# Kernel optimization log

Hardware: AMD Instinct MI355X
Metric: run time of the kernel (lower is better)

## Reference

```python
import jax, jax.numpy as jnp
import numpy as np

NEG_SLOPE = 0.2  # PyG GATv2Conv default negative_slope


def segment_softmax(scores, dst, num_nodes):
    # scores: [E, H], softmax over edges sharing the same destination node
    m = jax.ops.segment_max(scores, dst, num_segments=num_nodes)  # [N, H]
    e = jnp.exp(scores - m[dst])
    s = jax.ops.segment_sum(e, dst, num_segments=num_nodes)  # [N, H]
    return e / (s[dst] + 1e-16)


def gatv2_conv(x, src, dst, Wl, bl, Wr, br, att, bias, heads, out_ch, concat):
    # PyG GATv2: x_l = lin_l(x) used for source/messages, x_r = lin_r(x) for target
    n = x.shape[0]
    xl = (x @ Wl + bl).reshape(n, heads, out_ch)
    xr = (x @ Wr + br).reshape(n, heads, out_ch)
    e = jax.nn.leaky_relu(xl[src] + xr[dst], NEG_SLOPE)        # [E, H, C]
    score = jnp.einsum('ehc,hc->eh', e, att)                    # [E, H]
    alpha = segment_softmax(score, dst, n)                      # [E, H]
    msg = xl[src] * alpha[..., None]                            # [E, H, C]
    out = jax.ops.segment_sum(msg, dst, num_segments=n)         # [N, H, C]
    out = out.reshape(n, heads * out_ch) if concat else out.mean(axis=1)
    return out + bias


def setup_inputs() -> dict:
    key = jax.random.key(0)
    ks = jax.random.split(key, 20)
    N, F_IN, H, C = 50000, 256, 4, 64
    E = 600000
    x = jax.random.normal(ks[0], (N, F_IN), dtype=jnp.float32)
    edge_index = jax.random.randint(ks[1], (2, E), 0, N, dtype=jnp.int64)

    def glorot(k, shape):
        fan_in = shape[0]
        return jax.random.normal(k, shape, dtype=jnp.float32) / jnp.sqrt(jnp.float32(fan_in))

    params = dict(
        # layer 1: in=256, heads=4, out=64, concat -> 256
        W1l=glorot(ks[2], (F_IN, H * C)), b1l=jnp.zeros((H * C,), jnp.float32),
        W1r=glorot(ks[3], (F_IN, H * C)), b1r=jnp.zeros((H * C,), jnp.float32),
        att1=glorot(ks[4], (H, C)), bias1=jnp.zeros((H * C,), jnp.float32),
        # layer 2: in=256, heads=1, out=64, no concat
        W2l=glorot(ks[5], (H * C, C)), b2l=jnp.zeros((C,), jnp.float32),
        W2r=glorot(ks[6], (H * C, C)), b2r=jnp.zeros((C,), jnp.float32),
        att2=glorot(ks[7], (1, C)), bias2=jnp.zeros((C,), jnp.float32),
        # predict head: 64 -> 32 -> 1
        Wp1=glorot(ks[8], (C, 32)), bp1=jnp.zeros((32,), jnp.float32),
        Wp2=glorot(ks[9], (32, 1)), bp2=jnp.zeros((1,), jnp.float32),
    )
    return {'x': x, 'edge_index': edge_index, **params}


def reference(x, edge_index, W1l, b1l, W1r, b1r, att1, bias1,
              W2l, b2l, W2r, b2r, att2, bias2, Wp1, bp1, Wp2, bp2):
    n = x.shape[0]
    # PyG GATv2Conv default add_self_loops=True
    loop = jnp.arange(n, dtype=edge_index.dtype)
    src = jnp.concatenate([edge_index[0], loop])
    dst = jnp.concatenate([edge_index[1], loop])

    h = gatv2_conv(x, src, dst, W1l, b1l, W1r, b1r, att1, bias1,
                   heads=4, out_ch=64, concat=True)
    h = jax.nn.leaky_relu(h, 0.01)  # F.leaky_relu default slope
    h = gatv2_conv(h, src, dst, W2l, b2l, W2r, b2r, att2, bias2,
                   heads=1, out_ch=64, concat=False)
    z = jax.nn.leaky_relu(h @ Wp1 + bp1, 0.01)
    logits = z @ Wp2 + bp2
    return logits, h
```

## Files before the change

### kernel.cpp

```cpp
#include <hip/hip_runtime.h>

typedef __attribute__((ext_vector_type(8))) __bf16 bf16x8;
typedef __attribute__((ext_vector_type(4))) float f32x4;

#define EXP2 __builtin_amdgcn_exp2f
#define LOG2E 1.44269504f
#define MFMA __builtin_amdgcn_mfma_f32_16x16x32_bf16

#define GLL(srcp, dstp) __builtin_amdgcn_global_load_lds( \
    (const __attribute__((address_space(1))) void*)(srcp), \
    (__attribute__((address_space(3))) void*)(dstp), 16, 0, 0)

__device__ __forceinline__ float lrelu(float v, float s) { return v > 0.f ? v : v * s; }

__device__ __forceinline__ unsigned short f2bf(float f) {
    unsigned int u = __float_as_uint(f);
    u += 0x7FFFu + ((u >> 16) & 1u);
    return (unsigned short)(u >> 16);
}
__device__ __forceinline__ float bf2f(unsigned short u) {
    return __uint_as_float((unsigned int)u << 16);
}

__device__ __forceinline__ int ld_idx(const int* p, int e, int is64) {
    return is64 ? (int)(((const long long*)p)[e]) : p[e];
}

__global__ void detect_i64(const unsigned int* idx, int* flag) {
    if (blockIdx.x == 0 && threadIdx.x == 0) {
        int all0 = 1;
        for (int i = 1; i < 256; i += 2) {
            if (idx[i] != 0u) { all0 = 0; break; }
        }
        *flag = all0;
    }
}

__global__ void convert_all(const float* __restrict__ x,
                            const float* __restrict__ W1l, const float* __restrict__ W1r,
                            const float* __restrict__ W2l, const float* __restrict__ W2r,
                            unsigned short* __restrict__ xb,
                            unsigned short* __restrict__ w1t, unsigned short* __restrict__ w2t,
                            int n, int nrb)
{
    int t = blockIdx.x * blockDim.x + threadIdx.x;
    int A = nrb * 512;
    if (t < A) {
        int lane = t & 63;
        int kf = (t >> 6) & 7;
        int rowblk = t >> 9;
        int r16 = lane & 15, kg = lane >> 4;
        int row = rowblk * 16 + r16;
        int k0 = kf * 32 + kg * 8;
        ushort4 o0 = {0, 0, 0, 0}, o1 = {0, 0, 0, 0};
        if (row < n) {
            float4 v0 = *(const float4*)(x + (size_t)row * 256 + k0);
            float4 v1 = *(const float4*)(x + (size_t)row * 256 + k0 + 4);
            o0.x = f2bf(v0.x); o0.y = f2bf(v0.y); o0.z = f2bf(v0.z); o0.w = f2bf(v0.w);
            o1.x = f2bf(v1.x); o1.y = f2bf(v1.y); o1.z = f2bf(v1.z); o1.w = f2bf(v1.w);
        }
        *(ushort4*)(xb + (size_t)t * 8) = o0;
        *(ushort4*)(xb + (size_t)t * 8 + 4) = o1;
        return;
    }
    int tw = t - A;
    const float *Wl, *Wr;
    unsigned short* dst;
    int NL, base;
    if (tw < 16384)      { Wl = W1l; Wr = W1r; dst = w1t; NL = 256; base = tw; }
    else if (tw < 20480) { Wl = W2l; Wr = W2r; dst = w2t; NL = 64;  base = tw - 16384; }
    else return;
    int lane = base & 63, kf = (base >> 6) & 7, colblk = base >> 9;
    int r16 = lane & 15, kg = lane >> 4;
    int col = colblk * 16 + r16;
    int k0 = kf * 32 + kg * 8;
    const float* W = (col < NL) ? Wl : Wr;
    int c = (col < NL) ? col : col - NL;
    unsigned short v[8];
#pragma unroll
    for (int e = 0; e < 8; e++) v[e] = f2bf(W[(size_t)(k0 + e) * NL + c]);
    ushort4 o0 = {v[0], v[1], v[2], v[3]}, o1 = {v[4], v[5], v[6], v[7]};
    *(ushort4*)(dst + (size_t)base * 8) = o0;
    *(ushort4*)(dst + (size_t)base * 8 + 4) = o1;
}

template <int KF>
__global__ __launch_bounds__(256) void gemm_lds(
    const unsigned short* __restrict__ A, const unsigned short* __restrict__ Bt,
    const float* __restrict__ biasL, const float* __restrict__ biasR, int NL,
    unsigned short* __restrict__ C, int M, int nrb, int N)
{
    __shared__ unsigned short lds[2][16 * 512];
    int wid = threadIdx.x >> 6, lane = threadIdx.x & 63;
    int wm = wid >> 1, wn = wid & 1;
    int rb0 = blockIdx.x * 8;
    int cb0 = blockIdx.y * 8;

    auto stage = [&](int buf, int kf) {
#pragma unroll
        for (int i = 0; i < 4; i++) {
            int c = wid * 4 + i;
            const unsigned short* src;
            if (c < 8) {
                int rb = rb0 + c;
                rb = rb < nrb ? rb : nrb - 1;
                src = A + ((size_t)rb * KF + kf) * 512;
            } else {
                src = Bt + ((size_t)(cb0 + c - 8) * KF + kf) * 512;
            }
            GLL(src + lane * 8, &lds[buf][c * 512]);
        }
    };

    f32x4 acc[4][4] = {};
    stage(0, 0);
    __syncthreads();
    int cur = 0;
    for (int kf = 0; kf < KF; kf++) {
        if (kf + 1 < KF) stage(cur ^ 1, kf + 1);
        bf16x8 a[4], b[4];
#pragma unroll
        for (int r = 0; r < 4; r++)
            a[r] = *(const bf16x8*)&lds[cur][(wm * 4 + r) * 512 + lane * 8];
#pragma unroll
        for (int j = 0; j < 4; j++)
            b[j] = *(const bf16x8*)&lds[cur][(8 + wn * 4 + j) * 512 + lane * 8];
#pragma unroll
        for (int j = 0; j < 4; j++)
#pragma unroll
            for (int r = 0; r < 4; r++)
                acc[r][j] = MFMA(a[r], b[j], acc[r][j], 0, 0, 0);
        __syncthreads();
        cur ^= 1;
    }

    int ccol = lane & 15, crow = (lane >> 4) * 4;
#pragma unroll
    for (int r = 0; r < 4; r++) {
#pragma unroll
        for (int j = 0; j < 4; j++) {
            int col = (cb0 + wn * 4 + j) * 16 + ccol;
            float bv = (col < NL) ? biasL[col] : biasR[col - NL];
#pragma unroll
            for (int q = 0; q < 4; q++) {
                int row = (rb0 + wm * 4 + r) * 16 + crow + q;
                if (row < M) C[(size_t)row * N + col] = f2bf(acc[r][j][q] + bv);
            }
        }
    }
}

__global__ void hist_dst_pos(const int* __restrict__ eidx, const int* __restrict__ flagp,
                             int E, int n, int* __restrict__ cnt, int* __restrict__ pos)
{
    int t = blockIdx.x * blockDim.x + threadIdx.x;
    if (t >= E + n) return;
    int is64 = *flagp;
    int d = (t < E) ? ld_idx(eidx, E + t, is64) : (t - E);
    pos[t] = atomicAdd(&cnt[d], 1);
}

__global__ __launch_bounds__(1024) void scan1(const int* __restrict__ cnt,
                                              int* __restrict__ rowptr, int* __restrict__ psum, int n)
{
    __shared__ int wsum[16];
    int tid = threadIdx.x, lane = tid & 63, w = tid >> 6;
    int gid = blockIdx.x * 1024 + tid;
    int v = (gid < n) ? cnt[gid] : 0;
    int sc = v;
#pragma unroll
    for (int o = 1; o < 64; o <<= 1) { int t2 = __shfl_up(sc, o); if (lane >= o) sc += t2; }
    if (lane == 63) wsum[w] = sc;
    __syncthreads();
    if (tid < 16) {
        int t2 = wsum[tid];
#pragma unroll
        for (int o = 1; o < 16; o <<= 1) { int u = __shfl_up(t2, o); if (tid >= o) t2 += u; }
        wsum[tid] = t2;
    }
    __syncthreads();
    int wofs = w ? wsum[w - 1] : 0;
    if (gid < n) rowptr[gid] = wofs + sc - v;
    if (tid == 1023) psum[blockIdx.x] = wsum[15];
}

__global__ void scan2(const int* __restrict__ psum, int* __restrict__ pofs,
                      int* __restrict__ rowptr_n, int nb)
{
    int lane = threadIdx.x;
    int v = (lane < nb) ? psum[lane] : 0;
    int sc = v;
#pragma unroll
    for (int o = 1; o < 64; o <<= 1) { int t = __shfl_up(sc, o); if (lane >= o) sc += t; }
    if (lane < nb) pofs[lane] = sc - v;
    if (lane == 63) *rowptr_n = sc;
}

__global__ __launch_bounds__(1024) void scan3(int* __restrict__ rowptr,
                                              const int* __restrict__ pofs, int n)
{
    int gid = blockIdx.x * 1024 + threadIdx.x;
    if (gid < n) rowptr[gid] += pofs[blockIdx.x];
}

__global__ void scatter_pos(const int* __restrict__ eidx, const int* __restrict__ flagp,
                            int E, int n, const int* __restrict__ rowptr,
                            const int* __restrict__ pos, int* __restrict__ sord)
{
    int t = blockIdx.x * blockDim.x + threadIdx.x;
    if (t >= E + n) return;
    int is64 = *flagp;
    int s, d;
    if (t < E) { s = ld_idx(eidx, t, is64); d = ld_idx(eidx, E + t, is64); }
    else { s = t - E; d = s; }
    sord[rowptr[d] + pos[t]] = s;
}

#define SCOREX(p, xv) { float t_; p = 0.f;                              \
    t_ = xv.x + xrv.x; p = fmaf(t_, a6.x, p); p = fmaf(fabsf(t_), a4.x, p); \
    t_ = xv.y + xrv.y; p = fmaf(t_, a6.y, p); p = fmaf(fabsf(t_), a4.y, p); \
    t_ = xv.z + xrv.z; p = fmaf(t_, a6.z, p); p = fmaf(fabsf(t_), a4.z, p); \
    t_ = xv.w + xrv.w; p = fmaf(t_, a6.w, p); p = fmaf(fabsf(t_), a4.w, p); }

#define RED16(p) { p += __shfl_xor(p, 1); p += __shfl_xor(p, 2);    \
                   p += __shfl_xor(p, 4); p += __shfl_xor(p, 8); }

#define EACC(v, xv) { float ev = EXP2(v); ssum += ev;                \
    o.x = fmaf(ev, xv.x, o.x); o.y = fmaf(ev, xv.y, o.y);            \
    o.z = fmaf(ev, xv.z, o.z); o.w = fmaf(ev, xv.w, o.w); }

#define CVT4(f, u) float4 f = { bf2f(u.x), bf2f(u.y), bf2f(u.z), bf2f(u.w) };

__global__ __launch_bounds__(256) void node_attn_h4(
    const unsigned short* __restrict__ xlr,
    const float* __restrict__ att, const float* __restrict__ bias,
    const int* __restrict__ rowptr, const int* __restrict__ sord, int n,
    unsigned short* __restrict__ outb)
{
    int d = (blockIdx.x * blockDim.x + threadIdx.x) >> 6;
    int lane = threadIdx.x & 63;
    if (d >= n) return;
    int off = (lane >> 4) * 64 + (lane & 15) * 4;
    ushort4 xru = *(const ushort4*)(xlr + (size_t)d * 512 + 256 + off);
    CVT4(xrv, xru);
    float4 atv = *(const float4*)(att + off);
    float4 a6, a4;
    a6.x = atv.x * (0.6f * LOG2E); a6.y = atv.y * (0.6f * LOG2E);
    a6.z = atv.z * (0.6f * LOG2E); a6.w = atv.w * (0.6f * LOG2E);
    a4.x = atv.x * (0.4f * LOG2E); a4.y = atv.y * (0.4f * LOG2E);
    a4.z = atv.z * (0.4f * LOG2E); a4.w = atv.w * (0.4f * LOG2E);
    int beg = rowptr[d], end = rowptr[d + 1];
    float ssum = 0.f;
    float4 o = {0.f, 0.f, 0.f, 0.f};
    for (int i = beg; i < end; i += 4) {
        int i1 = i + 1, i2 = i + 2, i3 = i + 3;
        int v1 = i1 < end, v2 = i2 < end, v3 = i3 < end;
        int s0 = sord[i];
        int s1 = sord[v1 ? i1 : i];
        int s2 = sord[v2 ? i2 : i];
        int s3 = sord[v3 ? i3 : i];
        ushort4 u0 = *(const ushort4*)(xlr + (size_t)s0 * 512 + off);
        ushort4 u1 = *(const ushort4*)(xlr + (size_t)s1 * 512 + off);
        ushort4 u2 = *(const ushort4*)(xlr + (size_t)s2 * 512 + off);
        ushort4 u3 = *(const ushort4*)(xlr + (size_t)s3 * 512 + off);
        CVT4(x0, u0); CVT4(x1, u1); CVT4(x2, u2); CVT4(x3, u3);
        float p0, p1, p2, p3;
        SCOREX(p0, x0); SCOREX(p1, x1); SCOREX(p2, x2); SCOREX(p3, x3);
        RED16(p0); RED16(p1); RED16(p2); RED16(p3);
        p1 = v1 ? p1 : -1e30f;
        p2 = v2 ? p2 : -1e30f;
        p3 = v3 ? p3 : -1e30f;
        EACC(p0, x0); EACC(p1, x1); EACC(p2, x2); EACC(p3, x3);
    }
    float inv = 1.f / (ssum + 1e-16f);
    float4 bv = *(const float4*)(bias + off);
    float r0 = o.x * inv + bv.x, r1 = o.y * inv + bv.y;
    float r2 = o.z * inv + bv.z, r3 = o.w * inv + bv.w;
    r0 = fmaxf(r0, 0.01f * r0); r1 = fmaxf(r1, 0.01f * r1);
    r2 = fmaxf(r2, 0.01f * r2); r3 = fmaxf(r3, 0.01f * r3);
    ushort4 ov;
    ov.x = f2bf(r0); ov.y = f2bf(r1); ov.z = f2bf(r2); ov.w = f2bf(r3);
    int rowblk = d >> 4, r16d = d & 15;
    int kf = off >> 5, kg2 = (off >> 3) & 3, e0 = off & 7;
    size_t flat = (((size_t)rowblk * 8 + kf) * 64 + kg2 * 16 + r16d) * 8 + e0;
    *(ushort4*)(outb + flat) = ov;
}

__global__ __launch_bounds__(256) void node_attn_h1(
    const unsigned short* __restrict__ xlr,
    const float* __restrict__ att, const float* __restrict__ bias,
    const int* __restrict__ rowptr, const int* __restrict__ sord, int n,
    float* __restrict__ outf)
{
    int d = (blockIdx.x * blockDim.x + threadIdx.x) >> 6;
    int lane = threadIdx.x & 63;
    if (d >= n) return;
    int sg = lane >> 4, c0 = (lane & 15) * 4;
    ushort4 xru = *(const ushort4*)(xlr + (size_t)d * 128 + 64 + c0);
    CVT4(xrv, xru);
    float4 atv = *(const float4*)(att + c0);
    float4 a6, a4;
    a6.x = atv.x * (0.6f * LOG2E); a6.y = atv.y * (0.6f * LOG2E);
    a6.z = atv.z * (0.6f * LOG2E); a6.w = atv.w * (0.6f * LOG2E);
    a4.x = atv.x * (0.4f * LOG2E); a4.y = atv.y * (0.4f * LOG2E);
    a4.z = atv.z * (0.4f * LOG2E); a4.w = atv.w * (0.4f * LOG2E);
    int beg = rowptr[d], end = rowptr[d + 1];
    float ssum = 0.f;
    float4 o = {0.f, 0.f, 0.f, 0.f};
    for (int i0 = beg; i0 < end; i0 += 8) {
        int ia = i0 + sg, ib = i0 + 4 + sg;
        int va = ia < end, vb = ib < end;
        int sa = sord[va ? ia : beg];
        int sb = sord[vb ? ib : beg];
        ushort4 ua = *(const ushort4*)(xlr + (size_t)sa * 128 + c0);
        ushort4 ub = *(const ushort4*)(xlr + (size_t)sb * 128 + c0);
        CVT4(xa, ua); CVT4(xb, ub);
        float pa, pb;
        SCOREX(pa, xa); SCOREX(pb, xb);
        RED16(pa); RED16(pb);
        pa = va ? pa : -1e30f;
        pb = vb ? pb : -1e30f;
        EACC(pa, xa); EACC(pb, xb);
    }
#pragma unroll
    for (int offs = 16; offs <= 32; offs <<= 1) {
        ssum += __shfl_xor(ssum, offs);
        o.x += __shfl_xor(o.x, offs); o.y += __shfl_xor(o.y, offs);
        o.z += __shfl_xor(o.z, offs); o.w += __shfl_xor(o.w, offs);
    }
    if (sg == 0) {
        float inv = 1.f / (ssum + 1e-16f);
        float4 bv = *(const float4*)(bias + c0);
        float4 res;
        res.x = o.x * inv + bv.x; res.y = o.y * inv + bv.y;
        res.z = o.z * inv + bv.z; res.w = o.w * inv + bv.w;
        *(float4*)(outf + (size_t)d * 64 + c0) = res;
    }
}

__global__ void predict_head(const float* __restrict__ h2,
                             const float* __restrict__ Wp1, const float* __restrict__ bp1,
                             const float* __restrict__ Wp2, const float* __restrict__ bp2,
                             float* __restrict__ logits, int n)
{
    int i = blockIdx.x * blockDim.x + threadIdx.x;
    if (i >= n) return;
    float h[64];
#pragma unroll
    for (int c = 0; c < 64; c++) h[c] = h2[(long long)i * 64 + c];
    float logit = bp2[0];
#pragma unroll
    for (int j = 0; j < 32; j++) {
        float z = bp1[j];
#pragma unroll
        for (int c = 0; c < 64; c++) z += h[c] * Wp1[c * 32 + j];
        z = lrelu(z, 0.01f);
        logit += z * Wp2[j];
    }
    logits[i] = logit;
}

extern "C" void kernel_launch(void* const* d_in, const int* in_sizes, int n_in,
                              void* d_out, int out_size, void* d_ws, size_t ws_size,
                              hipStream_t stream)
{
    const float* x    = (const float*)d_in[0];
    const int*   eidx = (const int*)d_in[1];
    const float* W1l  = (const float*)d_in[2];
    const float* b1l  = (const float*)d_in[3];
    const float* W1r  = (const float*)d_in[4];
    const float* b1r  = (const float*)d_in[5];
    const float* att1 = (const float*)d_in[6];
    const float* bias1= (const float*)d_in[7];
    const float* W2l  = (const float*)d_in[8];
    const float* b2l  = (const float*)d_in[9];
    const float* W2r  = (const float*)d_in[10];
    const float* b2r  = (const float*)d_in[11];
    const float* att2 = (const float*)d_in[12];
    const float* bias2= (const float*)d_in[13];
    const float* Wp1  = (const float*)d_in[14];
    const float* bp1  = (const float*)d_in[15];
    const float* Wp2  = (const float*)d_in[16];
    const float* bp2  = (const float*)d_in[17];

    const int n = in_sizes[0] / 256;
    const int E = in_sizes[1] / 2;
    const int Etot = E + n;
    const int nb = (n + 1023) / 1024;
    const int nrb = (n + 15) / 16;

    float* out = (float*)d_out;
    unsigned short* ws16 = (unsigned short*)d_ws;

    unsigned short* xb    = ws16;
    unsigned short* xlr1  = xb + (size_t)nrb * 4096;
    unsigned short* w1t   = xlr1 + (size_t)n * 512;
    unsigned short* w2t   = w1t + 131072;
    int*            rowptr= (int*)(w2t + 32768);
    int*            cnt   = rowptr + (n + 1);
    int*            sord  = cnt + n;
    int*            pos   = sord + Etot;
    int*            psum  = pos + Etot;
    int*            pofs  = psum + 64;
    int*            flagp = pofs + 64;
    unsigned short* h1b   = xb;
    unsigned short* xlr2  = xlr1;
    float*          h2    = out + n;

    detect_i64<<<1, 64, 0, stream>>>((const unsigned int*)eidx, flagp);

    hipMemsetAsync(cnt, 0, (size_t)n * sizeof(int), stream);
    hist_dst_pos<<<(Etot + 255) / 256, 256, 0, stream>>>(eidx, flagp, E, n, cnt, pos);
    scan1<<<nb, 1024, 0, stream>>>(cnt, rowptr, psum, n);
    scan2<<<1, 64, 0, stream>>>(psum, pofs, rowptr + n, nb);
    scan3<<<nb, 1024, 0, stream>>>(rowptr, pofs, n);
    scatter_pos<<<(Etot + 255) / 256, 256, 0, stream>>>(eidx, flagp, E, n, rowptr, pos, sord);

    convert_all<<<(nrb * 512 + 20480 + 255) / 256, 256, 0, stream>>>(
        x, W1l, W1r, W2l, W2r, xb, w1t, w2t, n, nrb);

    {
        dim3 grid((nrb + 7) / 8, 4);
        gemm_lds<8><<<grid, 256, 0, stream>>>(xb, w1t, b1l, b1r, 256, xlr1, n, nrb, 512);
    }

    node_attn_h4<<<(n + 3) / 4, 256, 0, stream>>>(xlr1, att1, bias1, rowptr, sord, n, h1b);

    {
        dim3 grid((nrb + 7) / 8, 1);
        gemm_lds<8><<<grid, 256, 0, stream>>>(h1b, w2t, b2l, b2r, 64, xlr2, n, nrb, 128);
    }

    node_attn_h1<<<(n + 3) / 4, 256, 0, stream>>>(xlr2, att2, bias2, rowptr, sord, n, h2);

    predict_head<<<(n + 255) / 256, 256, 0, stream>>>(h2, Wp1, bp1, Wp2, bp2, out, n);
}
```

Measured before the change: 226.7 us.

## Remap GAT attention kernels to one wave per node with 8-channel lanes

Both per-node attention kernels now launch one 64-thread block per destination node. Each lane owns 8 contiguous channels, and the wave splits into slots that process different edges at the same time: 2 edges per iteration for the 4-head layer, 8 for the 1-head layer. Slot partials are combined with cross-slot shuffles at the end. The aim is wider per-lane loads, fewer score-reduction shuffles per edge and more edge parallelism. The trade-off is less per-lane unrolled ILP in the 4-head kernel, more loop iterations, and more small blocks.

After: 236.2 us. 1.04x slower.

```diff
diff --git a/kernel.cpp b/kernel.cpp
--- a/kernel.cpp
+++ b/kernel.cpp
@@ -216,125 +216,155 @@
     sord[rowptr[d] + pos[t]] = s;
 }
 
-#define SCOREX(p, xv) { float t_; p = 0.f;                              \
-    t_ = xv.x + xrv.x; p = fmaf(t_, a6.x, p); p = fmaf(fabsf(t_), a4.x, p); \
-    t_ = xv.y + xrv.y; p = fmaf(t_, a6.y, p); p = fmaf(fabsf(t_), a4.y, p); \
-    t_ = xv.z + xrv.z; p = fmaf(t_, a6.z, p); p = fmaf(fabsf(t_), a4.z, p); \
-    t_ = xv.w + xrv.w; p = fmaf(t_, a6.w, p); p = fmaf(fabsf(t_), a4.w, p); }
-
-#define RED16(p) { p += __shfl_xor(p, 1); p += __shfl_xor(p, 2);    \
-                   p += __shfl_xor(p, 4); p += __shfl_xor(p, 8); }
-
-#define EACC(v, xv) { float ev = EXP2(v); ssum += ev;                \
-    o.x = fmaf(ev, xv.x, o.x); o.y = fmaf(ev, xv.y, o.y);            \
-    o.z = fmaf(ev, xv.z, o.z); o.w = fmaf(ev, xv.w, o.w); }
-
-#define CVT4(f, u) float4 f = { bf2f(u.x), bf2f(u.y), bf2f(u.z), bf2f(u.w) };
-
-__global__ __launch_bounds__(256) void node_attn_h4(
+__global__ __launch_bounds__(64) void node_attn_h4(
     const unsigned short* __restrict__ xlr,
     const float* __restrict__ att, const float* __restrict__ bias,
     const int* __restrict__ rowptr, const int* __restrict__ sord, int n,
     unsigned short* __restrict__ outb)
 {
-    int d = (blockIdx.x * blockDim.x + threadIdx.x) >> 6;
-    int lane = threadIdx.x & 63;
-    if (d >= n) return;
-    int off = (lane >> 4) * 64 + (lane & 15) * 4;
-    ushort4 xru = *(const ushort4*)(xlr + (size_t)d * 512 + 256 + off);
-    CVT4(xrv, xru);
-    float4 atv = *(const float4*)(att + off);
-    float4 a6, a4;
-    a6.x = atv.x * (0.6f * LOG2E); a6.y = atv.y * (0.6f * LOG2E);
-    a6.z = atv.z * (0.6f * LOG2E); a6.w = atv.w * (0.6f * LOG2E);
-    a4.x = atv.x * (0.4f * LOG2E); a4.y = atv.y * (0.4f * LOG2E);
-    a4.z = atv.z * (0.4f * LOG2E); a4.w = atv.w * (0.4f * LOG2E);
+    int d = blockIdx.x;
+    int lane = threadIdx.x;
+    int slot = lane >> 5, sub = lane & 31;
+    int off = sub * 8;
+    float xr8[8], a68[8], a48[8];
+    {
+        ushort4 u0 = *(const ushort4*)(xlr + (size_t)d * 512 + 256 + off);
+        ushort4 u1 = *(const ushort4*)(xlr + (size_t)d * 512 + 256 + off + 4);
+        xr8[0] = bf2f(u0.x); xr8[1] = bf2f(u0.y); xr8[2] = bf2f(u0.z); xr8[3] = bf2f(u0.w);
+        xr8[4] = bf2f(u1.x); xr8[5] = bf2f(u1.y); xr8[6] = bf2f(u1.z); xr8[7] = bf2f(u1.w);
+        float4 av0 = *(const float4*)(att + off);
+        float4 av1 = *(const float4*)(att + off + 4);
+        float av[8] = {av0.x, av0.y, av0.z, av0.w, av1.x, av1.y, av1.z, av1.w};
+#pragma unroll
+        for (int c = 0; c < 8; c++) {
+            a68[c] = av[c] * (0.6f * LOG2E);
+            a48[c] = av[c] * (0.4f * LOG2E);
+        }
+    }
     int beg = rowptr[d], end = rowptr[d + 1];
     float ssum = 0.f;
-    float4 o = {0.f, 0.f, 0.f, 0.f};
-    for (int i = beg; i < end; i += 4) {
-        int i1 = i + 1, i2 = i + 2, i3 = i + 3;
-        int v1 = i1 < end, v2 = i2 < end, v3 = i3 < end;
-        int s0 = sord[i];
-        int s1 = sord[v1 ? i1 : i];
-        int s2 = sord[v2 ? i2 : i];
-        int s3 = sord[v3 ? i3 : i];
-        ushort4 u0 = *(const ushort4*)(xlr + (size_t)s0 * 512 + off);
-        ushort4 u1 = *(const ushort4*)(xlr + (size_t)s1 * 512 + off);
-        ushort4 u2 = *(const ushort4*)(xlr + (size_t)s2 * 512 + off);
-        ushort4 u3 = *(const ushort4*)(xlr + (size_t)s3 * 512 + off);
-        CVT4(x0, u0); CVT4(x1, u1); CVT4(x2, u2); CVT4(x3, u3);
-        float p0, p1, p2, p3;
-        SCOREX(p0, x0); SCOREX(p1, x1); SCOREX(p2, x2); SCOREX(p3, x3);
-        RED16(p0); RED16(p1); RED16(p2); RED16(p3);
-        p1 = v1 ? p1 : -1e30f;
-        p2 = v2 ? p2 : -1e30f;
-        p3 = v3 ? p3 : -1e30f;
-        EACC(p0, x0); EACC(p1, x1); EACC(p2, x2); EACC(p3, x3);
-    }
-    float inv = 1.f / (ssum + 1e-16f);
-    float4 bv = *(const float4*)(bias + off);
-    float r0 = o.x * inv + bv.x, r1 = o.y * inv + bv.y;
-    float r2 = o.z * inv + bv.z, r3 = o.w * inv + bv.w;
-    r0 = fmaxf(r0, 0.01f * r0); r1 = fmaxf(r1, 0.01f * r1);
-    r2 = fmaxf(r2, 0.01f * r2); r3 = fmaxf(r3, 0.01f * r3);
-    ushort4 ov;
-    ov.x = f2bf(r0); ov.y = f2bf(r1); ov.z = f2bf(r2); ov.w = f2bf(r3);
-    int rowblk = d >> 4, r16d = d & 15;
-    int kf = off >> 5, kg2 = (off >> 3) & 3, e0 = off & 7;
-    size_t flat = (((size_t)rowblk * 8 + kf) * 64 + kg2 * 16 + r16d) * 8 + e0;
-    *(ushort4*)(outb + flat) = ov;
-}
-
-__global__ __launch_bounds__(256) void node_attn_h1(
+    float o8[8] = {};
+    for (int i = beg; i < end; i += 2) {
+        int ia = i + slot;
+        int va = ia < end;
+        int sa = sord[va ? ia : i];
+        const unsigned short* rp = xlr + (size_t)sa * 512 + off;
+        ushort4 u0 = *(const ushort4*)rp;
+        ushort4 u1 = *(const ushort4*)(rp + 4);
+        float x8[8];
+        x8[0] = bf2f(u0.x); x8[1] = bf2f(u0.y); x8[2] = bf2f(u0.z); x8[3] = bf2f(u0.w);
+        x8[4] = bf2f(u1.x); x8[5] = bf2f(u1.y); x8[6] = bf2f(u1.z); x8[7] = bf2f(u1.w);
+        float p = 0.f;
+#pragma unroll
+        for (int c = 0; c < 8; c++) {
+            float t_ = x8[c] + xr8[c];
+            p = fmaf(t_, a68[c], p);
+            p = fmaf(fabsf(t_), a48[c], p);
+        }
+        p += __shfl_xor(p, 1);
+        p += __shfl_xor(p, 2);
+        p += __shfl_xor(p, 4);
+        p = va ? p : -1e30f;
+        float ev = EXP2(p);
+        ssum += ev;
+#pragma unroll
+        for (int c = 0; c < 8; c++) o8[c] = fmaf(ev, x8[c], o8[c]);
+    }
+    ssum += __shfl_xor(ssum, 32);
+#pragma unroll
+    for (int c = 0; c < 8; c++) o8[c] += __shfl_xor(o8[c], 32);
+    if (slot == 0) {
+        float inv = 1.f / (ssum + 1e-16f);
+        float4 bv0 = *(const float4*)(bias + off);
+        float4 bv1 = *(const float4*)(bias + off + 4);
+        float bv[8] = {bv0.x, bv0.y, bv0.z, bv0.w, bv1.x, bv1.y, bv1.z, bv1.w};
+        unsigned short r[8];
+#pragma unroll
+        for (int c = 0; c < 8; c++) {
+            float v = o8[c] * inv + bv[c];
+            v = fmaxf(v, 0.01f * v);
+            r[c] = f2bf(v);
+        }
+        int rowblk = d >> 4, r16d = d & 15;
+        int kf = off >> 5, kg = (off >> 3) & 3;
+        size_t flat = (((size_t)rowblk * 8 + kf) * 64 + kg * 16 + r16d) * 8;
+        ushort4 q0 = {r[0], r[1], r[2], r[3]}, q1 = {r[4], r[5], r[6], r[7]};
+        *(ushort4*)(outb + flat) = q0;
+        *(ushort4*)(outb + flat + 4) = q1;
+    }
+}
+
+__global__ __launch_bounds__(64) void node_attn_h1(
     const unsigned short* __restrict__ xlr,
     const float* __restrict__ att, const float* __restrict__ bias,
     const int* __restrict__ rowptr, const int* __restrict__ sord, int n,
     float* __restrict__ outf)
 {
-    int d = (blockIdx.x * blockDim.x + threadIdx.x) >> 6;
-    int lane = threadIdx.x & 63;
-    if (d >= n) return;
-    int sg = lane >> 4, c0 = (lane & 15) * 4;
-    ushort4 xru = *(const ushort4*)(xlr + (size_t)d * 128 + 64 + c0);
-    CVT4(xrv, xru);
-    float4 atv = *(const float4*)(att + c0);
-    float4 a6, a4;
-    a6.x = atv.x * (0.6f * LOG2E); a6.y = atv.y * (0.6f * LOG2E);
-    a6.z = atv.z * (0.6f * LOG2E); a6.w = atv.w * (0.6f * LOG2E);
-    a4.x = atv.x * (0.4f * LOG2E); a4.y = atv.y * (0.4f * LOG2E);
-    a4.z = atv.z * (0.4f * LOG2E); a4.w = atv.w * (0.4f * LOG2E);
+    int d = blockIdx.x;
+    int lane = threadIdx.x;
+    int slot = lane >> 3, sub = lane & 7;
+    int off = sub * 8;
+    float xr8[8], a68[8], a48[8];
+    {
+        ushort4 u0 = *(const ushort4*)(xlr + (size_t)d * 128 + 64 + off);
+        ushort4 u1 = *(const ushort4*)(xlr + (size_t)d * 128 + 64 + off + 4);
+        xr8[0] = bf2f(u0.x); xr8[1] = bf2f(u0.y); xr8[2] = bf2f(u0.z); xr8[3] = bf2f(u0.w);
+        xr8[4] = bf2f(u1.x); xr8[5] = bf2f(u1.y); xr8[6] = bf2f(u1.z); xr8[7] = bf2f(u1.w);
+        float4 av0 = *(const float4*)(att + off);
+        float4 av1 = *(const float4*)(att + off + 4);
+        float av[8] = {av0.x, av0.y, av0.z, av0.w, av1.x, av1.y, av1.z, av1.w};
+#pragma unroll
+        for (int c = 0; c < 8; c++) {
+            a68[c] = av[c] * (0.6f * LOG2E);
+            a48[c] = av[c] * (0.4f * LOG2E);
+        }
+    }
     int beg = rowptr[d], end = rowptr[d + 1];
     float ssum = 0.f;
-    float4 o = {0.f, 0.f, 0.f, 0.f};
-    for (int i0 = beg; i0 < end; i0 += 8) {
-        int ia = i0 + sg, ib = i0 + 4 + sg;
-        int va = ia < end, vb = ib < end;
-        int sa = sord[va ? ia : beg];
-        int sb = sord[vb ? ib : beg];
-        ushort4 ua = *(const ushort4*)(xlr + (size_t)sa * 128 + c0);
-        ushort4 ub = *(const ushort4*)(xlr + (size_t)sb * 128 + c0);
-        CVT4(xa, ua); CVT4(xb, ub);
-        float pa, pb;
-        SCOREX(pa, xa); SCOREX(pb, xb);
-        RED16(pa); RED16(pb);
-        pa = va ? pa : -1e30f;
-        pb = vb ? pb : -1e30f;
-        EACC(pa, xa); EACC(pb, xb);
-    }
-#pragma unroll
-    for (int offs = 16; offs <= 32; offs <<= 1) {
+    float o8[8] = {};
+    for (int i = beg; i < end; i += 8) {
+        int ia = i + slot;
+        int va = ia < end;
+        int sa = sord[va ? ia : i];
+        const unsigned short* rp = xlr + (size_t)sa * 128 + off;
+        ushort4 u0 = *(const ushort4*)rp;
+        ushort4 u1 = *(const ushort4*)(rp + 4);
+        float x8[8];
+        x8[0] = bf2f(u0.x); x8[1] = bf2f(u0.y); x8[2] = bf2f(u0.z); x8[3] = bf2f(u0.w);
+        x8[4] = bf2f(u1.x); x8[5] = bf2f(u1.y); x8[6] = bf2f(u1.z); x8[7] = bf2f(u1.w);
+        float p = 0.f;
+#pragma unroll
+        for (int c = 0; c < 8; c++) {
+            float t_ = x8[c] + xr8[c];
+            p = fmaf(t_, a68[c], p);
+            p = fmaf(fabsf(t_), a48[c], p);
+        }
+        p += __shfl_xor(p, 1);
+        p += __shfl_xor(p, 2);
+        p += __shfl_xor(p, 4);
+        p = va ? p : -1e30f;
+        float ev = EXP2(p);
+        ssum += ev;
+#pragma unroll
+        for (int c = 0; c < 8; c++) o8[c] = fmaf(ev, x8[c], o8[c]);
+    }
+#pragma unroll
+    for (int offs = 8; offs <= 32; offs <<= 1) {
         ssum += __shfl_xor(ssum, offs);
-        o.x += __shfl_xor(o.x, offs); o.y += __shfl_xor(o.y, offs);
-        o.z += __shfl_xor(o.z, offs); o.w += __shfl_xor(o.w, offs);
-    }
-    if (sg == 0) {
+#pragma unroll
+        for (int c = 0; c < 8; c++) o8[c] += __shfl_xor(o8[c], offs);
+    }
+    if (slot == 0) {
         float inv = 1.f / (ssum + 1e-16f);
-        float4 bv = *(const float4*)(bias + c0);
-        float4 res;
-        res.x = o.x * inv + bv.x; res.y = o.y * inv + bv.y;
-        res.z = o.z * inv + bv.z; res.w = o.w * inv + bv.w;
-        *(float4*)(outf + (size_t)d * 64 + c0) = res;
+        float4 bv0 = *(const float4*)(bias + off);
+        float4 bv1 = *(const float4*)(bias + off + 4);
+        float4 res0, res1;
+        res0.x = o8[0] * inv + bv0.x; res0.y = o8[1] * inv + bv0.y;
+        res0.z = o8[2] * inv + bv0.z; res0.w = o8[3] * inv + bv0.w;
+        res1.x = o8[4] * inv + bv1.x; res1.y = o8[5] * inv + bv1.y;
+        res1.z = o8[6] * inv + bv1.z; res1.w = o8[7] * inv + bv1.w;
+        *(float4*)(outf + (size_t)d * 64 + off) = res0;
+        *(float4*)(outf + (size_t)d * 64 + off + 4) = res1;
     }
 }
 
@@ -424,14 +454,14 @@
         gemm_lds<8><<<grid, 256, 0, stream>>>(xb, w1t, b1l, b1r, 256, xlr1, n, nrb, 512);
     }
 
-    node_attn_h4<<<(n + 3) / 4, 256, 0, stream>>>(xlr1, att1, bias1, rowptr, sord, n, h1b);
+    node_attn_h4<<<n, 64, 0, stream>>>(xlr1, att1, bias1, rowptr, sord, n, h1b);
 
     {
         dim3 grid((nrb + 7) / 8, 1);
         gemm_lds<8><<<grid, 256, 0, stream>>>(h1b, w2t, b2l, b2r, 64, xlr2, n, nrb, 128);
     }
 
-    node_attn_h1<<<(n + 3) / 4, 256, 0, stream>>>(xlr2, att2, bias2, rowptr, sord, n, h2);
+    node_attn_h1<<<n, 64, 0, stream>>>(xlr2, att2, bias2, rowptr, sord, n, h2);
 
     predict_head<<<(n + 255) / 256, 256, 0, stream>>>(h2, Wp1, bp1, Wp2, bp2, out, n);
 }
```
